# Performance work log

Hardware: AMD Instinct MI355X
Metric: run time of the kernel (lower is better)

Reference implementation:

```python
import jax, jax.numpy as jnp
import numpy as np

B, T, D, H, FC, A = 256, 128, 512, 1024, 1024, 32
LOG_STD_MIN, LOG_STD_MAX = -20.0, 2.0
EPS = 1e-5


def setup_inputs() -> dict:
    key = jax.random.key(0)
    ks = jax.random.split(key, 16)
    def w(k, shape, fan_in):
        return jax.random.normal(k, shape, jnp.float32) / np.float32(np.sqrt(fan_in))
    return {
        "observations": jax.random.normal(ks[0], (B, T, D), jnp.float32),
        "hidden_state": jax.random.normal(ks[1], (B, H), jnp.float32),
        "episode_starts": jax.random.randint(ks[2], (B, T), 0, 2, jnp.int32),
        "ln_gamma": jnp.ones((D,), jnp.float32),
        "ln_beta": jnp.zeros((D,), jnp.float32),
        "W_fc": w(ks[3], (FC, D), D), "b_fc": jnp.zeros((FC,), jnp.float32),
        "W_ih": w(ks[4], (3 * H, FC), FC), "b_ih": jnp.zeros((3 * H,), jnp.float32),
        "W_hh": w(ks[5], (3 * H, H), H), "b_hh": jnp.zeros((3 * H,), jnp.float32),
        "W_out": w(ks[6], (H, H), H), "b_out": jnp.zeros((H,), jnp.float32),
        "W_mean": w(ks[7], (A, H), H) * 0.01, "b_mean": jnp.zeros((A,), jnp.float32),
        "W_ls": w(ks[8], (A, H), H) * 0.01, "b_ls": jnp.zeros((A,), jnp.float32),
    }


def reference(observations, hidden_state, episode_starts, ln_gamma, ln_beta,
              W_fc, b_fc, W_ih, b_ih, W_hh, b_hh, W_out, b_out,
              W_mean, b_mean, W_ls, b_ls):
    # LayerNorm over last dim (eps=1e-5, like nn.LayerNorm)
    mu = jnp.mean(observations, axis=-1, keepdims=True)
    var = jnp.mean(jnp.square(observations - mu), axis=-1, keepdims=True)
    x = (observations - mu) * jax.lax.rsqrt(var + EPS) * ln_gamma + ln_beta
    # fc_in + ReLU, then precompute GRU input-gate projections for all steps
    x = jax.nn.relu(jnp.einsum('btd,fd->btf', x, W_fc) + b_fc)          # (B,T,FC)
    xg = jnp.einsum('btf,gf->btg', x, W_ih) + b_ih                      # (B,T,3H)
    xg_t = jnp.swapaxes(xg, 0, 1)                                       # (T,B,3H)
    starts_t = jnp.swapaxes(episode_starts, 0, 1).astype(jnp.float32)   # (T,B)

    def step(h, inp):
        xg_s, st = inp
        h = h * (1.0 - st)[:, None]
        gh = h @ W_hh.T + b_hh                                           # (B,3H)
        xr, xz, xn = xg_s[:, :H], xg_s[:, H:2 * H], xg_s[:, 2 * H:]
        hr, hz, hn = gh[:, :H], gh[:, H:2 * H], gh[:, 2 * H:]
        r = jax.nn.sigmoid(xr + hr)
        z = jax.nn.sigmoid(xz + hz)
        n = jnp.tanh(xn + r * hn)
        h_new = (1.0 - z) * n + z * h
        out = jax.nn.relu(h_new @ W_out.T + b_out)
        return h_new, out

    h_final, outs = jax.lax.scan(step, hidden_state, (xg_t, starts_t))
    feats = jnp.swapaxes(outs, 0, 1)                                     # (B,T,H)
    means = jnp.einsum('bth,ah->bta', feats, W_mean) + b_mean
    log_std = jnp.clip(jnp.einsum('bth,ah->bta', feats, W_ls) + b_ls,
                       LOG_STD_MIN, LOG_STD_MAX)
    return means, log_std, h_final
```

## Files before the change

kernel.cpp:

```cpp
#include <hip/hip_runtime.h>
#include <hip/hip_bf16.h>

#define B_ 256
#define T_ 128
#define D_ 512
#define H_ 1024
#define FC_ 1024
#define A_ 32
#define NWG_ 256

typedef short bf16x8 __attribute__((ext_vector_type(8)));
typedef float f32x4 __attribute__((ext_vector_type(4)));
typedef unsigned long long ull;

__device__ __forceinline__ float bf2f(unsigned short u) {
  return __uint_as_float(((unsigned)u) << 16);
}
__device__ __forceinline__ unsigned short f2bf(float x) {
  unsigned u = __float_as_uint(x);
  u = u + 0x7fffu + ((u >> 16) & 1u);
  return (unsigned short)(u >> 16);
}
__device__ __forceinline__ void unpack8(uint4 v, float* f) {
  f[0] = bf2f(v.x & 0xffff); f[1] = bf2f(v.x >> 16);
  f[2] = bf2f(v.y & 0xffff); f[3] = bf2f(v.y >> 16);
  f[4] = bf2f(v.z & 0xffff); f[5] = bf2f(v.z >> 16);
  f[6] = bf2f(v.w & 0xffff); f[7] = bf2f(v.w >> 16);
}
__device__ __forceinline__ uint4 pack8(const float* f) {
  uint4 v;
  v.x = (unsigned)f2bf(f[0]) | ((unsigned)f2bf(f[1]) << 16);
  v.y = (unsigned)f2bf(f[2]) | ((unsigned)f2bf(f[3]) << 16);
  v.z = (unsigned)f2bf(f[4]) | ((unsigned)f2bf(f[5]) << 16);
  v.w = (unsigned)f2bf(f[6]) | ((unsigned)f2bf(f[7]) << 16);
  return v;
}

__global__ __launch_bounds__(256) void detect_kernel(
    const unsigned short* __restrict__ obs, int* __restrict__ flag)
{
  __shared__ int cnt;
  if (threadIdx.x == 0) cnt = 0;
  __syncthreads();
  int c = 0;
  for (int i = threadIdx.x; i < 8192; i += 256) {
    unsigned e = (obs[i] >> 7) & 0xffu;
    if (e >= 0x86u) c++;
  }
  atomicAdd(&cnt, c);
  __syncthreads();
  if (threadIdx.x == 0) *flag = (cnt >= 64) ? 1 : 0;
}

struct CanonArgs {
  const void* src[14];
  unsigned short* dst[14];
  int ofs[15];
};
__global__ __launch_bounds__(256) void canon_kernel(CanonArgs a,
                                                    const int* __restrict__ flag)
{
  const int fl = *flag;
  const int i0 = (blockIdx.x * 256 + threadIdx.x) * 8;
  int t = 0;
  while (t < 14 && i0 >= a.ofs[t + 1]) t++;
  if (t >= 14) return;
  const int local = i0 - a.ofs[t];
  unsigned short* d = a.dst[t] + local;
  if (fl) {
    const float* s = (const float*)a.src[t] + local;
    #pragma unroll
    for (int e = 0; e < 8; e++) d[e] = f2bf(s[e]);
  } else {
    const unsigned short* s = (const unsigned short*)a.src[t] + local;
    #pragma unroll
    for (int e = 0; e < 8; e++) d[e] = s[e];
  }
}

__global__ __launch_bounds__(256) void ln_kernel(
    const void* __restrict__ obs,
    const unsigned short* __restrict__ gamma_,
    const unsigned short* __restrict__ beta_,
    unsigned short* __restrict__ xn, int t0, int tcShift,
    const int* __restrict__ flag)
{
  const int fl = *flag;
  const int lane = threadIdx.x & 63;
  const int rloc = blockIdx.x * 4 + (threadIdx.x >> 6);
  const int b  = rloc >> tcShift;
  const int tl = rloc & ((1 << tcShift) - 1);
  const int grow = b * T_ + t0 + tl;
  float f[8];
  if (fl) {
    const float* of = (const float*)obs + (size_t)grow * D_ + lane * 8;
    const float4 v0 = *(const float4*)of;
    const float4 v1 = *(const float4*)(of + 4);
    f[0] = v0.x; f[1] = v0.y; f[2] = v0.z; f[3] = v0.w;
    f[4] = v1.x; f[5] = v1.y; f[6] = v1.z; f[7] = v1.w;
  } else {
    uint4 v = *(const uint4*)((const unsigned short*)obs + (size_t)grow * D_ + lane * 8);
    unpack8(v, f);
  }
  float s = 0.f, ss = 0.f;
  #pragma unroll
  for (int i = 0; i < 8; i++) { s += f[i]; ss += f[i] * f[i]; }
  #pragma unroll
  for (int off = 32; off > 0; off >>= 1) {
    s  += __shfl_xor(s,  off, 64);
    ss += __shfl_xor(ss, off, 64);
  }
  const float mu  = s * (1.0f / D_);
  const float var = ss * (1.0f / D_) - mu * mu;
  const float inv = rsqrtf(var + 1e-5f);
  float g[8], b8[8];
  unpack8(*(const uint4*)(gamma_ + lane * 8), g);
  unpack8(*(const uint4*)(beta_  + lane * 8), b8);
  float o[8];
  #pragma unroll
  for (int i = 0; i < 8; i++) o[i] = (f[i] - mu) * inv * g[i] + b8[i];
  *(uint4*)(xn + (size_t)rloc * D_ + lane * 8) = pack8(o);
}

__global__ __launch_bounds__(256) void gemm_tn(
    const unsigned short* __restrict__ A, const unsigned short* __restrict__ Bm,
    const unsigned short* __restrict__ bias, unsigned short* __restrict__ C,
    int M, int N, int K, int relu)
{
  __shared__ short As[128 * 32];
  __shared__ short Bs[128 * 32];
  const int tid  = threadIdx.x;
  const int wave = tid >> 6, lane = tid & 63;
  const int quad = lane >> 4, l15 = lane & 15;
  const int m0 = blockIdx.y * 128, n0 = blockIdx.x * 128;
  const int wm = (wave >> 1) * 64, wn = (wave & 1) * 64;
  const int srow = tid >> 2;
  const int skc  = (tid & 3) * 8;
  const size_t aoff0 = (size_t)(m0 + srow) * K + skc;
  const size_t aoff1 = (size_t)(m0 + 64 + srow) * K + skc;
  const size_t boff0 = (size_t)(n0 + srow) * K + skc;
  const size_t boff1 = (size_t)(n0 + 64 + srow) * K + skc;
  const int lb0 = wave * 512;
  const int lb1 = 2048 + wave * 512;
  f32x4 acc[4][4] = {};
  for (int k0 = 0; k0 < K; k0 += 32) {
    __syncthreads();
    __builtin_amdgcn_global_load_lds(
        (const __attribute__((address_space(1))) unsigned*)(A + aoff0 + k0),
        (__attribute__((address_space(3))) unsigned*)&As[lb0], 16, 0, 0);
    __builtin_amdgcn_global_load_lds(
        (const __attribute__((address_space(1))) unsigned*)(A + aoff1 + k0),
        (__attribute__((address_space(3))) unsigned*)&As[lb1], 16, 0, 0);
    __builtin_amdgcn_global_load_lds(
        (const __attribute__((address_space(1))) unsigned*)(Bm + boff0 + k0),
        (__attribute__((address_space(3))) unsigned*)&Bs[lb0], 16, 0, 0);
    __builtin_amdgcn_global_load_lds(
        (const __attribute__((address_space(1))) unsigned*)(Bm + boff1 + k0),
        (__attribute__((address_space(3))) unsigned*)&Bs[lb1], 16, 0, 0);
    __syncthreads();
    bf16x8 af[4], bfv[4];
    #pragma unroll
    for (int i = 0; i < 4; i++) af[i]  = *(const bf16x8*)&As[(wm + i * 16 + l15) * 32 + quad * 8];
    #pragma unroll
    for (int j = 0; j < 4; j++) bfv[j] = *(const bf16x8*)&Bs[(wn + j * 16 + l15) * 32 + quad * 8];
    #pragma unroll
    for (int i = 0; i < 4; i++)
      #pragma unroll
      for (int j = 0; j < 4; j++)
        acc[i][j] = __builtin_amdgcn_mfma_f32_16x16x32_bf16(af[i], bfv[j], acc[i][j], 0, 0, 0);
  }
  #pragma unroll
  for (int j = 0; j < 4; j++) {
    const int col = n0 + wn + j * 16 + l15;
    const float bj = bias ? bf2f(bias[col]) : 0.0f;
    #pragma unroll
    for (int i = 0; i < 4; i++) {
      const int row = m0 + wm + i * 16 + quad * 4;
      #pragma unroll
      for (int r = 0; r < 4; r++) {
        float v = acc[i][j][r] + bj;
        if (relu) v = fmaxf(v, 0.0f);
        C[(size_t)(row + r) * N + col] = f2bf(v);
      }
    }
  }
}

__global__ __launch_bounds__(256, 1) void gru_scan(
    const unsigned short* __restrict__ xg,
    const int* __restrict__ starts,
    const unsigned short* __restrict__ Whh,
    const unsigned short* __restrict__ bhh,
    float* __restrict__ hf,
    ull* __restrict__ hb0,
    ull* __restrict__ hb1,
    unsigned short* __restrict__ hall,
    int t0, int Tc,
    int* __restrict__ flags)
{
  __shared__ short Ws[3 * 16 * 1032];
  __shared__ short Hs[2 * 64 * 136];
  __shared__ unsigned sbits[64][4];
  const int tid  = threadIdx.x;
  const int wg   = blockIdx.x;
  const int jb   = wg & 63, bb = wg >> 6;
  const int j0   = jb * 16, b0 = bb * 64;
  const int wave = tid >> 6, lane = tid & 63;
  const int quad = lane >> 4, l15 = lane & 15;

  for (int c = tid; c < 48 * 128; c += 256) {
    const int row = c >> 7;
    const int kc  = (c & 127) * 8;
    const int g = row >> 4, jj = row & 15;
    *(uint4*)&Ws[row * 1032 + kc] =
        *(const uint4*)(Whh + (size_t)(g * H_ + j0 + jj) * H_ + kc);
  }
  for (int c = tid; c < 64 * 4; c += 256) {
    const int row = c >> 2, w = c & 3;
    unsigned m = 0;
    #pragma unroll
    for (int bi = 0; bi < 32; bi++)
      m |= (starts[(b0 + row) * T_ + w * 32 + bi] ? 1u : 0u) << bi;
    sbits[row][w] = m;
  }
  const float br = bf2f(bhh[j0 + l15]);
  const float bz = bf2f(bhh[H_ + j0 + l15]);
  const float bn = bf2f(bhh[2 * H_ + j0 + l15]);
  const int col = j0 + l15;

  const int r0 = wave * 16 + quad * 4;
  float hreg[4];
  #pragma unroll
  for (int r = 0; r < 4; r++)
    hreg[r] = hf[(size_t)(b0 + r0 + r) * H_ + col];

  const int srow0 = tid >> 5;
  const int scol  = tid & 31;
  const size_t hbg = (size_t)(b0 + srow0) * 256 + scol;
  const int hsW = srow0 * 136 + scol * 4;
  const int hsR = (wave * 16 + l15) * 136 + quad * 8;
  const short* wsb = &Ws[l15 * 1032 + quad * 8];

  __syncthreads();

#define GRU_RBAR                                                              \
  { __builtin_amdgcn_sched_barrier(0); __builtin_amdgcn_s_barrier();          \
    __builtin_amdgcn_sched_barrier(0); }
#define GRU_LGKM0                                                             \
  { asm volatile("s_waitcnt lgkmcnt(0)" ::: "memory");                        \
    __builtin_amdgcn_sched_barrier(0); }

#define GRU_LOADC(dst, ch)                                                    \
  { _Pragma("unroll")                                                         \
    for (int u = 0; u < 8; u++)                                               \
      dst[u] = __hip_atomic_load(hin + hbg + u * 2048 + (ch) * 32,            \
                                 __ATOMIC_RELAXED, __HIP_MEMORY_SCOPE_AGENT); }

#define GRU_WRITE(src, s)                                                     \
  { _Pragma("unroll")                                                         \
    for (int u = 0; u < 8; u++) {                                             \
      ull v = src[u];                                                         \
      if ((sbits[srow0 + u * 8][tw] >> tb) & 1u) v = 0ull;                    \
      *(ull*)&Hs[(s) * 8704 + hsW + u * 1088] = v;                            \
    } }

#define GRU_MFMA2(p)                                                          \
  { _Pragma("unroll")                                                         \
    for (int w4 = 0; w4 < 4; w4++) {                                          \
      const bf16x8 a = *(const bf16x8*)&Hs[hsR + w4 * 32];                    \
      acc[0] = __builtin_amdgcn_mfma_f32_16x16x32_bf16(                       \
          a, *(const bf16x8*)(wsb + 0 * 16512 + ((2*(p))*4 + w4) * 32),       \
          acc[0], 0, 0, 0);                                                   \
      acc[1] = __builtin_amdgcn_mfma_f32_16x16x32_bf16(                       \
          a, *(const bf16x8*)(wsb + 1 * 16512 + ((2*(p))*4 + w4) * 32),       \
          acc[1], 0, 0, 0);                                                   \
      acc[2] = __builtin_amdgcn_mfma_f32_16x16x32_bf16(                       \
          a, *(const bf16x8*)(wsb + 2 * 16512 + ((2*(p))*4 + w4) * 32),       \
          acc[2], 0, 0, 0);                                                   \
    }                                                                         \
    _Pragma("unroll")                                                         \
    for (int w4 = 0; w4 < 4; w4++) {                                          \
      const bf16x8 a = *(const bf16x8*)&Hs[8704 + hsR + w4 * 32];             \
      acc[0] = __builtin_amdgcn_mfma_f32_16x16x32_bf16(                       \
          a, *(const bf16x8*)(wsb + 0 * 16512 + ((2*(p)+1)*4 + w4) * 32),     \
          acc[0], 0, 0, 0);                                                   \
      acc[1] = __builtin_amdgcn_mfma_f32_16x16x32_bf16(                       \
          a, *(const bf16x8*)(wsb + 1 * 16512 + ((2*(p)+1)*4 + w4) * 32),     \
          acc[1], 0, 0, 0);                                                   \
      acc[2] = __builtin_amdgcn_mfma_f32_16x16x32_bf16(                       \
          a, *(const bf16x8*)(wsb + 2 * 16512 + ((2*(p)+1)*4 + w4) * 32),     \
          acc[2], 0, 0, 0);                                                   \
    } }

  for (int tl = 0; tl < Tc; tl++) {
    const int t = t0 + tl;
    const ull* hin = (t & 1) ? hb1 : hb0;
    unsigned* hout_u = (unsigned*)((t & 1) ? hb0 : hb1);
    const unsigned tw = (unsigned)(t >> 5), tb = (unsigned)(t & 31);

    ull pfA0[8], pfA1[8], pfB0[8], pfB1[8];
    GRU_LOADC(pfA0, 0) GRU_LOADC(pfA1, 1)
    GRU_LOADC(pfB0, 2) GRU_LOADC(pfB1, 3)

    float xr[4], xz[4], xnv[4];
    #pragma unroll
    for (int r = 0; r < 4; r++) {
      const size_t xrow = ((size_t)(b0 + r0 + r) * Tc + tl) * (3 * H_);
      xr[r]  = bf2f(xg[xrow + col]);
      xz[r]  = bf2f(xg[xrow + H_ + col]);
      xnv[r] = bf2f(xg[xrow + 2 * H_ + col]);
    }

    f32x4 acc[3] = {};
    GRU_WRITE(pfA0, 0) GRU_WRITE(pfA1, 1)
    GRU_LGKM0
    GRU_RBAR
    GRU_LOADC(pfA0, 4) GRU_LOADC(pfA1, 5)
    GRU_MFMA2(0)
    GRU_RBAR
    GRU_WRITE(pfB0, 0) GRU_WRITE(pfB1, 1)
    GRU_LGKM0
    GRU_RBAR
    GRU_LOADC(pfB0, 6) GRU_LOADC(pfB1, 7)
    GRU_MFMA2(1)
    GRU_RBAR
    GRU_WRITE(pfA0, 0) GRU_WRITE(pfA1, 1)
    GRU_LGKM0
    GRU_RBAR
    GRU_MFMA2(2)
    GRU_RBAR
    GRU_WRITE(pfB0, 0) GRU_WRITE(pfB1, 1)
    GRU_LGKM0
    GRU_RBAR
    GRU_MFMA2(3)

    #pragma unroll
    for (int r = 0; r < 4; r++) {
      const int lrow = r0 + r;
      const int b = b0 + lrow;
      const float kb = ((sbits[lrow][tw] >> tb) & 1u) ? 0.0f : 1.0f;
      const float hr = acc[0][r] + br;
      const float hz = acc[1][r] + bz;
      const float hn = acc[2][r] + bn;
      const float rg = 1.0f / (1.0f + __expf(-(xr[r] + hr)));
      const float zg = 1.0f / (1.0f + __expf(-(xz[r] + hz)));
      const float ng = tanhf(xnv[r] + rg * hn);
      const float hv = (1.0f - zg) * ng + zg * (hreg[r] * kb);
      hreg[r] = hv;
      const unsigned mine = (unsigned)f2bf(hv);
      const unsigned other = (unsigned)__shfl_xor((int)mine, 1, 64);
      if ((l15 & 1) == 0) {
        const unsigned packed = mine | (other << 16);
        __hip_atomic_store(&hout_u[((size_t)b * H_ + col) >> 1], packed,
                           __ATOMIC_RELAXED, __HIP_MEMORY_SCOPE_AGENT);
        ((unsigned*)hall)[(((size_t)b * Tc + tl) * H_ + col) >> 1] = packed;
      }
    }

    const int my = t0 + tl + 1;
    __builtin_amdgcn_s_waitcnt(0);
    __syncthreads();
    if (tid == 0)
      __hip_atomic_store(&flags[wg * 32], my, __ATOMIC_RELAXED,
                         __HIP_MEMORY_SCOPE_AGENT);
    if (tid < 64) {
      while (__hip_atomic_load(&flags[(bb * 64 + tid) * 32], __ATOMIC_RELAXED,
                               __HIP_MEMORY_SCOPE_AGENT) < my)
        __builtin_amdgcn_s_sleep(1);
    }
    __syncthreads();
  }
#undef GRU_LOADC
#undef GRU_WRITE
#undef GRU_MFMA2
#undef GRU_RBAR
#undef GRU_LGKM0

  #pragma unroll
  for (int r = 0; r < 4; r++)
    hf[(size_t)(b0 + r0 + r) * H_ + col] = hreg[r];
}

__global__ __launch_bounds__(256) void heads_kernel(
    const unsigned short* __restrict__ feats,
    const unsigned short* __restrict__ Wm, const unsigned short* __restrict__ bm,
    const unsigned short* __restrict__ Wl, const unsigned short* __restrict__ bl,
    void* __restrict__ outbuf, int t0, int tcShift, const int* __restrict__ flag)
{
  __shared__ short Fs[64][40];
  __shared__ short Ws[64][40];
  const int fl = *flag;
  const int tid  = threadIdx.x;
  const int wave = tid >> 6, lane = tid & 63;
  const int quad = lane >> 4, l15 = lane & 15;
  const int m0 = blockIdx.x * 64;
  const int lrow = tid >> 2, lk = (tid & 3) * 8;
  f32x4 acc[4] = {};
  for (int k0 = 0; k0 < H_; k0 += 32) {
    __syncthreads();
    *(uint4*)&Fs[lrow][lk] = *(const uint4*)(feats + (size_t)(m0 + lrow) * H_ + k0 + lk);
    const unsigned short* wsrc = (lrow < 32)
        ? (Wm + (size_t)lrow * H_ + k0 + lk)
        : (Wl + (size_t)(lrow - 32) * H_ + k0 + lk);
    *(uint4*)&Ws[lrow][lk] = *(const uint4*)wsrc;
    __syncthreads();
    bf16x8 af = *(const bf16x8*)&Fs[wave * 16 + l15][quad * 8];
    #pragma unroll
    for (int j = 0; j < 4; j++) {
      bf16x8 bfv = *(const bf16x8*)&Ws[j * 16 + l15][quad * 8];
      acc[j] = __builtin_amdgcn_mfma_f32_16x16x32_bf16(af, bfv, acc[j], 0, 0, 0);
    }
  }
  const int tcMask = (1 << tcShift) - 1;
  const size_t lstdBase = (size_t)B_ * T_ * A_;
  #pragma unroll
  for (int j = 0; j < 4; j++) {
    const int col = j * 16 + l15;
    #pragma unroll
    for (int r = 0; r < 4; r++) {
      const int row = m0 + wave * 16 + quad * 4 + r;
      const int grow = (row >> tcShift) * T_ + t0 + (row & tcMask);
      float v = acc[j][r];
      size_t idx;
      if (col < 32) {
        v += bf2f(bm[col]);
        idx = (size_t)grow * A_ + col;
      } else {
        v += bf2f(bl[col - 32]);
        v = fminf(fmaxf(v, -20.0f), 2.0f);
        idx = lstdBase + (size_t)grow * A_ + (col - 32);
      }
      if (fl) ((float*)outbuf)[idx] = v;
      else    ((unsigned short*)outbuf)[idx] = f2bf(v);
    }
  }
}

__global__ __launch_bounds__(256) void h0_cast(const void* __restrict__ h0,
                                               float* __restrict__ hf,
                                               unsigned short* __restrict__ hb0,
                                               const int* __restrict__ flag) {
  const int fl = *flag;
  int i = blockIdx.x * 256 + threadIdx.x;
  float v = fl ? ((const float*)h0)[i] : bf2f(((const unsigned short*)h0)[i]);
  hf[i] = v;
  hb0[i] = f2bf(v);
}
__global__ __launch_bounds__(256) void hfin_store(const float* __restrict__ h,
                                                  void* __restrict__ outbuf,
                                                  const int* __restrict__ flag) {
  const int fl = *flag;
  const size_t base = 2ull * B_ * T_ * A_;
  int i = blockIdx.x * 256 + threadIdx.x;
  if (fl) ((float*)outbuf)[base + i] = h[i];
  else    ((unsigned short*)outbuf)[base + i] = f2bf(h[i]);
}

extern "C" void kernel_launch(void* const* d_in, const int* in_sizes, int n_in,
                              void* d_out, int out_size, void* d_ws, size_t ws_size,
                              hipStream_t stream)
{
  const void* obs    = d_in[0];
  const void* h0in   = d_in[1];
  const int*  starts = (const int*)d_in[2];
  const void* fsrc[14] = { d_in[5], d_in[7], d_in[9], d_in[11], d_in[13], d_in[15],
                           d_in[3], d_in[4], d_in[6], d_in[8], d_in[10], d_in[12],
                           d_in[14], d_in[16] };
  const int fn[14] = { FC_ * D_, 3 * H_ * FC_, 3 * H_ * H_, H_ * H_, A_ * H_, A_ * H_,
                       D_, D_, FC_, 3 * H_, 3 * H_, H_, A_, A_ };

  char* ws = (char*)d_ws;
  int* flag = (int*)ws;
  size_t cur = 256;
  unsigned short* cdst[14];
  for (int i = 0; i < 14; i++) {
    cdst[i] = (unsigned short*)(ws + cur);
    cur += (size_t)fn[i] * 2;
    cur = (cur + 255) & ~255ull;
  }
  const size_t chunkBase = cur;
  const size_t fixedTail = 1048576ull  + 2ull * 524288ull
                         + 32768ull ;

  int Tc = 1;
  for (int c = 32; c >= 1; c >>= 1) {
    size_t need = chunkBase + (size_t)c * 2883584ull + fixedTail;
    if (need <= ws_size) { Tc = c; break; }
  }
  int tcShift = 0;
  while ((1 << tcShift) < Tc) tcShift++;

  unsigned short* xn   = (unsigned short*)(ws + chunkBase);
  unsigned short* xfc  = (unsigned short*)(ws + chunkBase + (size_t)Tc * 262144ull);
  unsigned short* xg   = (unsigned short*)(ws + chunkBase + (size_t)Tc * 786432ull);
  unsigned short* hall = (unsigned short*)(ws + chunkBase + (size_t)Tc * 2359296ull);
  size_t o = chunkBase + (size_t)Tc * 2883584ull;
  float* hf           = (float*)(ws + o);           o += 1048576ull;
  unsigned short* hb0 = (unsigned short*)(ws + o);  o += 524288ull;
  unsigned short* hb1 = (unsigned short*)(ws + o);  o += 524288ull;
  int* flags          = (int*)(ws + o);
  unsigned short* feats = xg;

  const unsigned short *Wfc = cdst[0], *Wih = cdst[1], *Whh = cdst[2], *Wout = cdst[3];
  const unsigned short *Wmean = cdst[4], *Wls = cdst[5];
  const unsigned short *gam = cdst[6], *bet = cdst[7], *bfc = cdst[8], *bih = cdst[9];
  const unsigned short *bhh = cdst[10], *bout = cdst[11], *bmean = cdst[12], *bls = cdst[13];

  detect_kernel<<<dim3(1), dim3(256), 0, stream>>>((const unsigned short*)obs, flag);
  CanonArgs ca;
  int total = 0;
  for (int i = 0; i < 14; i++) {
    ca.src[i] = fsrc[i];
    ca.dst[i] = cdst[i];
    ca.ofs[i] = total;
    total += fn[i];
  }
  ca.ofs[14] = total;
  canon_kernel<<<dim3((total / 8 + 255) / 256), dim3(256), 0, stream>>>(ca, flag);
  h0_cast<<<dim3(B_ * H_ / 256), dim3(256), 0, stream>>>(h0in, hf, hb0, flag);
  hipMemsetAsync(flags, 0, 32768, stream);

  const int Mc = B_ * Tc;
  for (int t0 = 0; t0 < T_; t0 += Tc) {
    ln_kernel<<<dim3(Mc / 4), dim3(256), 0, stream>>>(obs, gam, bet, xn, t0, tcShift, flag);
    gemm_tn<<<dim3(FC_ / 128, Mc / 128), dim3(256), 0, stream>>>(
        xn, Wfc, bfc, xfc, Mc, FC_, D_, 1);
    gemm_tn<<<dim3(3 * H_ / 128, Mc / 128), dim3(256), 0, stream>>>(
        xfc, Wih, bih, xg, Mc, 3 * H_, FC_, 0);

    gru_scan<<<dim3(NWG_), dim3(256), 0, stream>>>(
        xg, starts, Whh, bhh, hf,
        (ull*)hb0, (ull*)hb1,
        hall, t0, Tc, flags);

    gemm_tn<<<dim3(H_ / 128, Mc / 128), dim3(256), 0, stream>>>(
        hall, Wout, bout, feats, Mc, H_, H_, 1);
    heads_kernel<<<dim3(Mc / 64), dim3(256), 0, stream>>>(
        feats, Wmean, bmean, Wls, bls, d_out, t0, tcShift, flag);
  }

  hfin_store<<<dim3(B_ * H_ / 256), dim3(256), 0, stream>>>(hf, d_out, flag);
}
```

Measured before the change: 1.745 ms.

## Use per-XCD cache invalidation with plain loads and a full-grid barrier in GRU scan

```diff
diff --git a/kernel.cpp b/kernel.cpp
--- a/kernel.cpp
+++ b/kernel.cpp
@@ -207,6 +207,11 @@
   const int j0   = jb * 16, b0 = bb * 64;
   const int wave = tid >> 6, lane = tid & 63;
   const int quad = lane >> 4, l15 = lane & 15;
+  int* aux = flags + 8192;
+
+  unsigned xcd;
+  asm volatile("s_getreg_b32 %0, hwreg(HW_REG_XCC_ID)" : "=s"(xcd));
+  xcd &= 7u;
 
   for (int c = tid; c < 48 * 128; c += 256) {
     const int row = c >> 7;
@@ -253,8 +258,7 @@
 #define GRU_LOADC(dst, ch)                                                    \
   { _Pragma("unroll")                                                         \
     for (int u = 0; u < 8; u++)                                               \
-      dst[u] = __hip_atomic_load(hin + hbg + u * 2048 + (ch) * 32,            \
-                                 __ATOMIC_RELAXED, __HIP_MEMORY_SCOPE_AGENT); }
+      dst[u] = *(const ull*)(hin + hbg + u * 2048 + (ch) * 32); }
 
 #define GRU_WRITE(src, s)                                                     \
   { _Pragma("unroll")                                                         \
@@ -298,6 +302,28 @@
     unsigned* hout_u = (unsigned*)((t & 1) ? hb0 : hb1);
     const unsigned tw = (unsigned)(t >> 5), tb = (unsigned)(t & 31);
 
+    {
+      const int tgt = t + 1;
+      if (tid == 0) {
+        int* claim = aux + xcd * 32;
+        int* idone = aux + (8 + xcd) * 32;
+        if (atomicMax(claim, tgt) < tgt) {
+          __builtin_amdgcn_fence(__ATOMIC_ACQUIRE, "agent");
+          asm volatile("s_waitcnt vmcnt(0)" ::: "memory");
+          __hip_atomic_store(idone, tgt, __ATOMIC_RELAXED,
+                             __HIP_MEMORY_SCOPE_AGENT);
+        } else {
+          while (__hip_atomic_load(idone, __ATOMIC_RELAXED,
+                                   __HIP_MEMORY_SCOPE_AGENT) < tgt)
+            __builtin_amdgcn_s_sleep(1);
+        }
+      }
+      __syncthreads();
+      asm volatile("buffer_inv" ::: "memory");
+      asm volatile("s_waitcnt vmcnt(0)" ::: "memory");
+      __builtin_amdgcn_sched_barrier(0);
+    }
+
     ull pfA0[8], pfA1[8], pfB0[8], pfB1[8];
     GRU_LOADC(pfA0, 0) GRU_LOADC(pfA1, 1)
     GRU_LOADC(pfB0, 2) GRU_LOADC(pfB1, 3)
@@ -363,11 +389,9 @@
     if (tid == 0)
       __hip_atomic_store(&flags[wg * 32], my, __ATOMIC_RELAXED,
                          __HIP_MEMORY_SCOPE_AGENT);
-    if (tid < 64) {
-      while (__hip_atomic_load(&flags[(bb * 64 + tid) * 32], __ATOMIC_RELAXED,
-                               __HIP_MEMORY_SCOPE_AGENT) < my)
-        __builtin_amdgcn_s_sleep(1);
-    }
+    while (__hip_atomic_load(&flags[tid * 32], __ATOMIC_RELAXED,
+                             __HIP_MEMORY_SCOPE_AGENT) < my)
+      __builtin_amdgcn_s_sleep(1);
     __syncthreads();
   }
 #undef GRU_LOADC
@@ -480,7 +504,7 @@
   }
   const size_t chunkBase = cur;
   const size_t fixedTail = 1048576ull  + 2ull * 524288ull
-                         + 32768ull ;
+                         + 36864ull ;
 
   int Tc = 1;
   for (int c = 32; c >= 1; c >>= 1) {
@@ -518,7 +542,7 @@
   ca.ofs[14] = total;
   canon_kernel<<<dim3((total / 8 + 255) / 256), dim3(256), 0, stream>>>(ca, flag);
   h0_cast<<<dim3(B_ * H_ / 256), dim3(256), 0, stream>>>(h0in, hf, hb0, flag);
-  hipMemsetAsync(flags, 0, 32768, stream);
+  hipMemsetAsync(flags, 0, 36864, stream);
 
   const int Mc = B_ * Tc;
   for (int t0 = 0; t0 < T_; t0 += Tc) {
```

Result: slower. 1.867 ms (+7.0%).

## Replace per-step flag barrier with sentinel-tagged hidden-state ring buffer

Applied to the files above, without the earlier changes.

```diff
diff --git a/kernel.cpp b/kernel.cpp
--- a/kernel.cpp
+++ b/kernel.cpp
@@ -192,11 +192,9 @@
     const unsigned short* __restrict__ Whh,
     const unsigned short* __restrict__ bhh,
     float* __restrict__ hf,
-    ull* __restrict__ hb0,
-    ull* __restrict__ hb1,
+    unsigned short* __restrict__ hb,
     unsigned short* __restrict__ hall,
-    int t0, int Tc,
-    int* __restrict__ flags)
+    int t0, int Tc)
 {
   __shared__ short Ws[3 * 16 * 1032];
   __shared__ short Hs[2 * 64 * 136];
@@ -240,6 +238,8 @@
   const int hsW = srow0 * 136 + scol * 4;
   const int hsR = (wave * 16 + l15) * 136 + quad * 8;
   const short* wsb = &Ws[l15 * 1032 + quad * 8];
+  const ull* hbull = (const ull*)hb;
+  unsigned* hbu32 = (unsigned*)hb;
 
   __syncthreads();
 
@@ -250,11 +250,28 @@
   { asm volatile("s_waitcnt lgkmcnt(0)" ::: "memory");                        \
     __builtin_amdgcn_sched_barrier(0); }
 
-#define GRU_LOADC(dst, ch)                                                    \
+#define GRU_ISSUE(dst, ch)                                                    \
   { _Pragma("unroll")                                                         \
     for (int u = 0; u < 8; u++)                                               \
       dst[u] = __hip_atomic_load(hin + hbg + u * 2048 + (ch) * 32,            \
                                  __ATOMIC_RELAXED, __HIP_MEMORY_SCOPE_AGENT); }
+
+#define GRU_OK8(x) ((((unsigned)(x)) != 0xC1C1C1C1u) &&                       \
+                    (((unsigned)((x) >> 32)) != 0xC1C1C1C1u))
+
+#define GRU_SPINV(dst, ch)                                                    \
+  { for (;;) {                                                                \
+      int ok = 1;                                                             \
+      _Pragma("unroll")                                                       \
+      for (int u = 0; u < 8; u++) ok &= (int)GRU_OK8(dst[u]);                 \
+      if (__all(ok)) break;                                                   \
+      __builtin_amdgcn_s_sleep(1);                                            \
+      _Pragma("unroll")                                                       \
+      for (int u = 0; u < 8; u++)                                             \
+        dst[u] = __hip_atomic_load(hin + hbg + u * 2048 + (ch) * 32,          \
+                                   __ATOMIC_RELAXED,                          \
+                                   __HIP_MEMORY_SCOPE_AGENT);                 \
+    } }
 
 #define GRU_WRITE(src, s)                                                     \
   { _Pragma("unroll")                                                         \
@@ -294,13 +311,14 @@
 
   for (int tl = 0; tl < Tc; tl++) {
     const int t = t0 + tl;
-    const ull* hin = (t & 1) ? hb1 : hb0;
-    unsigned* hout_u = (unsigned*)((t & 1) ? hb0 : hb1);
+    const ull* hin   = hbull + (size_t)((t + 3) & 3) * 65536;
+    unsigned* hout_u = hbu32 + (size_t)(t & 3) * 131072;
+    unsigned* hsent  = hbu32 + (size_t)((t + 2) & 3) * 131072;
     const unsigned tw = (unsigned)(t >> 5), tb = (unsigned)(t & 31);
 
-    ull pfA0[8], pfA1[8], pfB0[8], pfB1[8];
-    GRU_LOADC(pfA0, 0) GRU_LOADC(pfA1, 1)
-    GRU_LOADC(pfB0, 2) GRU_LOADC(pfB1, 3)
+    ull pf0[8], pf1[8], pf2[8], pf3[8];
+    GRU_ISSUE(pf0, 0) GRU_ISSUE(pf1, 1)
+    GRU_ISSUE(pf2, 2) GRU_ISSUE(pf3, 3)
 
     float xr[4], xz[4], xnv[4];
     #pragma unroll
@@ -312,26 +330,38 @@
     }
 
     f32x4 acc[3] = {};
-    GRU_WRITE(pfA0, 0) GRU_WRITE(pfA1, 1)
+    GRU_SPINV(pf0, 0) GRU_SPINV(pf1, 1)
+    GRU_RBAR
+    GRU_WRITE(pf0, 0) GRU_WRITE(pf1, 1)
     GRU_LGKM0
     GRU_RBAR
-    GRU_LOADC(pfA0, 4) GRU_LOADC(pfA1, 5)
+    GRU_ISSUE(pf0, 4) GRU_ISSUE(pf1, 5)
     GRU_MFMA2(0)
-    GRU_RBAR
-    GRU_WRITE(pfB0, 0) GRU_WRITE(pfB1, 1)
+    GRU_SPINV(pf2, 2) GRU_SPINV(pf3, 3)
+    GRU_RBAR
+    GRU_WRITE(pf2, 0) GRU_WRITE(pf3, 1)
     GRU_LGKM0
     GRU_RBAR
-    GRU_LOADC(pfB0, 6) GRU_LOADC(pfB1, 7)
+    GRU_ISSUE(pf2, 6) GRU_ISSUE(pf3, 7)
     GRU_MFMA2(1)
-    GRU_RBAR
-    GRU_WRITE(pfA0, 0) GRU_WRITE(pfA1, 1)
+    GRU_SPINV(pf0, 4) GRU_SPINV(pf1, 5)
+    GRU_RBAR
+    GRU_WRITE(pf0, 0) GRU_WRITE(pf1, 1)
     GRU_LGKM0
     GRU_RBAR
     GRU_MFMA2(2)
-    GRU_RBAR
-    GRU_WRITE(pfB0, 0) GRU_WRITE(pfB1, 1)
+    GRU_SPINV(pf2, 6) GRU_SPINV(pf3, 7)
+    GRU_RBAR
+    GRU_WRITE(pf2, 0) GRU_WRITE(pf3, 1)
     GRU_LGKM0
     GRU_RBAR
+    #pragma unroll
+    for (int r = 0; r < 4; r++) {
+      if ((l15 & 1) == 0)
+        __hip_atomic_store(&hsent[((size_t)(b0 + r0 + r) * H_ + col) >> 1],
+                           0xC1C1C1C1u, __ATOMIC_RELAXED,
+                           __HIP_MEMORY_SCOPE_AGENT);
+    }
     GRU_MFMA2(3)
 
     #pragma unroll
@@ -350,27 +380,16 @@
       const unsigned mine = (unsigned)f2bf(hv);
       const unsigned other = (unsigned)__shfl_xor((int)mine, 1, 64);
       if ((l15 & 1) == 0) {
-        const unsigned packed = mine | (other << 16);
+        unsigned packed = mine | (other << 16);
+        if (packed == 0xC1C1C1C1u) packed ^= 1u;
         __hip_atomic_store(&hout_u[((size_t)b * H_ + col) >> 1], packed,
                            __ATOMIC_RELAXED, __HIP_MEMORY_SCOPE_AGENT);
         ((unsigned*)hall)[(((size_t)b * Tc + tl) * H_ + col) >> 1] = packed;
       }
     }
-
-    const int my = t0 + tl + 1;
-    __builtin_amdgcn_s_waitcnt(0);
-    __syncthreads();
-    if (tid == 0)
-      __hip_atomic_store(&flags[wg * 32], my, __ATOMIC_RELAXED,
-                         __HIP_MEMORY_SCOPE_AGENT);
-    if (tid < 64) {
-      while (__hip_atomic_load(&flags[(bb * 64 + tid) * 32], __ATOMIC_RELAXED,
-                               __HIP_MEMORY_SCOPE_AGENT) < my)
-        __builtin_amdgcn_s_sleep(1);
-    }
-    __syncthreads();
-  }
-#undef GRU_LOADC
+  }
+#undef GRU_ISSUE
+#undef GRU_SPINV
 #undef GRU_WRITE
 #undef GRU_MFMA2
 #undef GRU_RBAR
@@ -438,13 +457,15 @@
 
 __global__ __launch_bounds__(256) void h0_cast(const void* __restrict__ h0,
                                                float* __restrict__ hf,
-                                               unsigned short* __restrict__ hb0,
+                                               unsigned short* __restrict__ hb3,
                                                const int* __restrict__ flag) {
   const int fl = *flag;
   int i = blockIdx.x * 256 + threadIdx.x;
   float v = fl ? ((const float*)h0)[i] : bf2f(((const unsigned short*)h0)[i]);
   hf[i] = v;
-  hb0[i] = f2bf(v);
+  unsigned short u = f2bf(v);
+  if (u == 0xC1C1) u ^= 1;
+  hb3[i] = u;
 }
 __global__ __launch_bounds__(256) void hfin_store(const float* __restrict__ h,
                                                   void* __restrict__ outbuf,
@@ -479,8 +500,7 @@
     cur = (cur + 255) & ~255ull;
   }
   const size_t chunkBase = cur;
-  const size_t fixedTail = 1048576ull  + 2ull * 524288ull
-                         + 32768ull ;
+  const size_t fixedTail = 1048576ull  + 2097152ull ;
 
   int Tc = 1;
   for (int c = 32; c >= 1; c >>= 1) {
@@ -495,10 +515,8 @@
   unsigned short* xg   = (unsigned short*)(ws + chunkBase + (size_t)Tc * 786432ull);
   unsigned short* hall = (unsigned short*)(ws + chunkBase + (size_t)Tc * 2359296ull);
   size_t o = chunkBase + (size_t)Tc * 2883584ull;
-  float* hf           = (float*)(ws + o);           o += 1048576ull;
-  unsigned short* hb0 = (unsigned short*)(ws + o);  o += 524288ull;
-  unsigned short* hb1 = (unsigned short*)(ws + o);  o += 524288ull;
-  int* flags          = (int*)(ws + o);
+  float* hf          = (float*)(ws + o);           o += 1048576ull;
+  unsigned short* hb = (unsigned short*)(ws + o);
   unsigned short* feats = xg;
 
   const unsigned short *Wfc = cdst[0], *Wih = cdst[1], *Whh = cdst[2], *Wout = cdst[3];
@@ -517,8 +535,9 @@
   }
   ca.ofs[14] = total;
   canon_kernel<<<dim3((total / 8 + 255) / 256), dim3(256), 0, stream>>>(ca, flag);
-  h0_cast<<<dim3(B_ * H_ / 256), dim3(256), 0, stream>>>(h0in, hf, hb0, flag);
-  hipMemsetAsync(flags, 0, 32768, stream);
+  hipMemsetAsync(hb, 0xC1, 2097152, stream);
+  h0_cast<<<dim3(B_ * H_ / 256), dim3(256), 0, stream>>>(
+      h0in, hf, hb + 3ull * 262144ull, flag);
 
   const int Mc = B_ * Tc;
   for (int t0 = 0; t0 < T_; t0 += Tc) {
@@ -529,9 +548,7 @@
         xfc, Wih, bih, xg, Mc, 3 * H_, FC_, 0);
 
     gru_scan<<<dim3(NWG_), dim3(256), 0, stream>>>(
-        xg, starts, Whh, bhh, hf,
-        (ull*)hb0, (ull*)hb1,
-        hall, t0, Tc, flags);
+        xg, starts, Whh, bhh, hf, hb, hall, t0, Tc);
 
     gemm_tn<<<dim3(H_ / 128, Mc / 128), dim3(256), 0, stream>>>(
         hall, Wout, bout, feats, Mc, H_, H_, 1);
```

Result: slower. 1.930 ms (+10.6%).
